# Kernel tuning notes

Measured on AMD Instinct MI355X. Metric: run time of the kernel, lower is better.

The kernel has to match this reference:

```python
import jax, jax.numpy as jnp
import numpy as np


def setup_inputs() -> dict:
    key = jax.random.key(0)
    k1, k2, k3, k4 = jax.random.split(key, 4)
    B, I, P, F = 4096, 1024, 512, 2048
    x = jax.random.normal(k1, (B, I), dtype=jnp.float32)
    # params initialized like torch.rand(...)*2-1 (uniform in [-1,1])
    features = jax.random.uniform(k2, (F, I), dtype=jnp.float32, minval=-1.0, maxval=1.0)
    prototypes = jax.random.uniform(k3, (P, I), dtype=jnp.float32, minval=-1.0, maxval=1.0)
    # scalars: torch inits to zeros; use small nonzero values so output/grads are informative
    abt = jax.random.normal(k4, (3,), dtype=jnp.float32) * 0.1
    alpha = abt[0:1]
    beta = abt[1:2]
    theta = abt[2:3]
    return {"x": x, "features": features, "prototypes": prototypes,
            "alpha": alpha, "beta": beta, "theta": theta}


def reference(x, features, prototypes, alpha, beta, theta):
    # x: [b, i], features: [f, i], prototypes: [p, i]
    # Original einsums broadcast over p but the projection is p-independent:
    xf = x @ features.T            # [b, f]
    pf = prototypes @ features.T   # [p, f]
    x_pres = jax.nn.relu(xf)       # [b, f]
    p_pres = jax.nn.relu(pf)       # [p, f]
    # common[b,p]       = sum_f xf*pf*relu(xf)*relu(pf)
    # x_distinct[b,p]   = sum_f xf*relu(xf)*(1-relu(pf))
    # p_distinct[b,p]   = sum_f pf*relu(pf)*(1-relu(xf))
    a = xf * x_pres                # [b, f]
    c = pf * p_pres                # [p, f]
    common = a @ c.T                                   # [b, p]
    x_distinctive = a @ (1.0 - p_pres).T               # [b, p]
    p_distinctive = (1.0 - x_pres) @ c.T               # [b, p]
    return theta * common - alpha * x_distinctive - beta * p_distinctive
```

## Files before the change

kernel.cpp:

```cpp
#include <hip/hip_runtime.h>
#include <cstdint>

typedef __attribute__((ext_vector_type(8))) short bf16x8;
typedef __attribute__((ext_vector_type(16))) float f32x16;
typedef __attribute__((ext_vector_type(4))) float f4;
typedef __attribute__((ext_vector_type(8))) unsigned short u16x8;
typedef unsigned short u16;


__device__ __forceinline__ u16 f2bf(float f) {
  uint32_t u = __builtin_bit_cast(uint32_t, f);
  u += 0x7fffu + ((u >> 16) & 1u);
  return (u16)(u >> 16);
}

__device__ __forceinline__ float bf2f(u16 h) {
  return __builtin_bit_cast(float, (uint32_t)h << 16);
}

__device__ __forceinline__ void async_cp16(const void* g, void* l) {
  __builtin_amdgcn_global_load_lds(
      (const __attribute__((address_space(1))) uint32_t*)g,
      (__attribute__((address_space(3))) uint32_t*)l, 16, 0, 0);
}

__global__ __launch_bounds__(256) void cast3(
    const float* __restrict__ x, const float* __restrict__ f,
    const float* __restrict__ p, u16* __restrict__ dst,
    int n1, int n2, int n3) {
  int i = (blockIdx.x * 256 + threadIdx.x) * 8;
  const float* src;
  int local;
  if (i < n1) { src = x; local = i; }
  else if (i < n1 + n2) { src = f; local = i - n1; }
  else if (i < n1 + n2 + n3) { src = p; local = i - n1 - n2; }
  else return;
  f4 a = *(const f4*)(src + local);
  f4 b = *(const f4*)(src + local + 4);
  u16x8 o;
  o[0] = f2bf(a.x); o[1] = f2bf(a.y); o[2] = f2bf(a.z); o[3] = f2bf(a.w);
  o[4] = f2bf(b.x); o[5] = f2bf(b.y); o[6] = f2bf(b.z); o[7] = f2bf(b.w);
  *(u16x8*)(dst + i) = o;
}


__device__ __forceinline__ void stage_tile(
    const u16* __restrict__ A, const u16* __restrict__ B, int K,
    int k0, int tid, u16* L) {
  constexpr int TM = 128, TN = 128;
  const int wave = tid >> 6;
  #pragma unroll
  for (int it = 0; it < TM / 32; ++it) {
    int c = it * 256 + tid;
    int row = c >> 3, pc = c & 7;
    int gc = pc ^ (row & 7);
    async_cp16(A + (size_t)row * K + (k0 + gc * 8),
               &L[(it * 256 + wave * 64) * 8]);
  }
  #pragma unroll
  for (int it = 0; it < TN / 32; ++it) {
    int c = it * 256 + tid;
    int row = c >> 3, pc = c & 7;
    int gc = pc ^ (row & 7);
    async_cp16(B + (size_t)row * K + (k0 + gc * 8),
               &L[TM * 64 + (it * 256 + wave * 64) * 8]);
  }
}

__device__ __forceinline__ void compute_tile(
    const u16* L, int lane, int wrow, int wcol, f32x16 (&acc)[2][2]) {
  constexpr int TM = 128;
  #pragma unroll
  for (int s = 0; s < 4; ++s) {
    const int h = s * 2 + (lane >> 5);
    bf16x8 bfr[2], afr[2];
    #pragma unroll
    for (int j = 0; j < 2; ++j) {
      const int rb = wcol * 64 + j * 32 + (lane & 31);
      bfr[j] = *(const bf16x8*)&L[TM * 64 + (rb * 8 + (h ^ (rb & 7))) * 8];
    }
    #pragma unroll
    for (int i = 0; i < 2; ++i) {
      const int ra = wrow * 64 + i * 32 + (lane & 31);
      afr[i] = *(const bf16x8*)&L[(ra * 8 + (h ^ (ra & 7))) * 8];
    }
    #pragma unroll
    for (int i = 0; i < 2; ++i)
      #pragma unroll
      for (int j = 0; j < 2; ++j)
        acc[i][j] = __builtin_amdgcn_mfma_f32_32x32x16_bf16(
            afr[i], bfr[j], acc[i][j], 0, 0, 0);
  }
}

__device__ __forceinline__ void mainloop(
    const u16* __restrict__ A, const u16* __restrict__ B, int K,
    int kbeg, int kend, int tid, u16* lds, f32x16 (&acc)[2][2]) {
  constexpr int BK = 64;
  constexpr int BUF = 16384;
  const int lane = tid & 63;
  const int wave = tid >> 6;
  const int wrow = wave >> 1, wcol = wave & 1;

  stage_tile(A, B, K, kbeg, tid, lds);
  int cur = 0;
  for (int k0 = kbeg; k0 < kend; k0 += BK) {
    if (k0 + BK < kend) {
      stage_tile(A, B, K, k0 + BK, tid, lds + (cur ^ 1) * BUF);
      asm volatile("s_waitcnt vmcnt(8)" ::: "memory");
    } else {
      asm volatile("s_waitcnt vmcnt(0)" ::: "memory");
    }
    __builtin_amdgcn_s_barrier();
    compute_tile(lds + cur * BUF, lane, wrow, wcol, acc);
    __builtin_amdgcn_s_barrier();
    cur ^= 1;
  }
}

__device__ __forceinline__ void mainloop_sb(
    const u16* __restrict__ A, const u16* __restrict__ B, int K,
    int kbeg, int kend, int tid, u16* lds, f32x16 (&acc)[2][2]) {
  constexpr int BK = 64;
  const int lane = tid & 63;
  const int wave = tid >> 6;
  const int wrow = wave >> 1, wcol = wave & 1;

  for (int k0 = kbeg; k0 < kend; k0 += BK) {
    stage_tile(A, B, K, k0, tid, lds);
    __syncthreads();
    compute_tile(lds, lane, wrow, wcol, acc);
    __syncthreads();
  }
}


__global__ __launch_bounds__(256) void gemm12(
    const u16* __restrict__ xb, const u16* __restrict__ pb,
    const u16* __restrict__ fb, u16* __restrict__ Acat, u16* __restrict__ Bcat,
    const float* __restrict__ alpha, const float* __restrict__ beta,
    const float* __restrict__ theta) {
  constexpr int TM = 128, K = 1024, N = 2048;
  constexpr int TSTRIDE = 136;
  __shared__ u16 lds[32768];

  const int tid = threadIdx.x;
  const int lane = tid & 63;
  const int wave = tid >> 6;
  const int wrow = wave >> 1, wcol = wave & 1;

  const int bid = blockIdx.x;
  const int xcd = bid & 7, slot = bid >> 3;
  const int xt = (xcd & 3) * 9 + (slot >> 3);
  const int yt = (xcd >> 2) * 8 + (slot & 7);

  const int bm_all = xt * TM;
  const int bn = yt * 128;
  const bool is_x = bm_all < 4096;
  const u16* A = is_x ? xb + (size_t)bm_all * K : pb + (size_t)(bm_all - 4096) * K;
  const u16* B = fb + (size_t)bn * K;

  f32x16 acc[2][2] = {};
  mainloop(A, B, K, 0, K, tid, lds, acc);

  float th = 0.f, al = 0.f, be = 0.f;
  if (!is_x) { th = theta[0]; al = alpha[0]; be = beta[0]; }
  u16* dst = is_x ? Acat : Bcat;
  const int rowbase = is_x ? bm_all : bm_all - 4096;
  const int rquad = 4 * (lane >> 5);

  #pragma unroll
  for (int half = 0; half < 2; ++half) {
    __syncthreads();
    #pragma unroll
    for (int i = 0; i < 2; ++i) {
      #pragma unroll
      for (int j = 0; j < 2; ++j) {
        const int cl = wcol * 64 + j * 32 + (lane & 31);
        #pragma unroll
        for (int r = 0; r < 16; ++r) {
          const int rl = wrow * 64 + i * 32 + (r & 3) + 8 * (r >> 2) + rquad;
          float v = acc[i][j][r];
          float pres = v > 0.f ? v : 0.f;
          float o;
          if (is_x) o = half == 0 ? v * pres : 1.f - pres;
          else {
            float cc = v * pres;
            o = half == 0 ? th * cc - al * (1.f - pres) : -be * cc;
          }
          lds[rl * TSTRIDE + cl] = f2bf(o);
        }
      }
    }
    __syncthreads();
    #pragma unroll
    for (int v = 0; v < 8; ++v) {
      const int rl = v * 16 + (tid >> 4);
      const int c8 = (tid & 15) * 8;
      u16x8 vec = *(const u16x8*)&lds[rl * TSTRIDE + c8];
      *(u16x8*)&dst[(size_t)(rowbase + rl) * (2 * N) + bn + c8 + half * N] = vec;
    }
  }
}

__global__ __launch_bounds__(256) void gemm3(
    const u16* __restrict__ Acat, const u16* __restrict__ Bcat,
    u16* __restrict__ part) {
  constexpr int TM = 128, TN = 128, K = 4096, KSPLIT = 8;
  __shared__ u16 lds[16384];

  const int tid = threadIdx.x;

  const int bid = blockIdx.x;
  const int bz = bid & 7;
  const int slot = bid >> 3;
  const int bxt = slot & 31;
  const int byt = slot >> 5;

  const int bm = bxt * TM;
  const int bn = byt * TN;
  const int kbeg = bz * (K / KSPLIT);
  const int kend = kbeg + (K / KSPLIT);

  f32x16 acc[2][2] = {};
  mainloop_sb(Acat + (size_t)bm * K, Bcat + (size_t)bn * K, K, kbeg, kend,
              tid, lds, acc);

  const size_t pbase = ((size_t)bz * 128 + byt * 32 + bxt) * 16384;
  #pragma unroll
  for (int i = 0; i < 2; ++i)
    #pragma unroll
    for (int j = 0; j < 2; ++j)
      #pragma unroll
      for (int h = 0; h < 2; ++h) {
        u16x8 o;
        #pragma unroll
        for (int e = 0; e < 8; ++e) o[e] = f2bf(acc[i][j][h * 8 + e]);
        *(u16x8*)&part[pbase + (size_t)(i * 4 + j * 2 + h) * 2048 + tid * 8] = o;
      }
}

__global__ __launch_bounds__(256) void reduce4(
    const u16* __restrict__ part, float* __restrict__ out) {
  constexpr int N = 512;
  const int tid = threadIdx.x;
  const int lane = tid & 63;
  const int wave = tid >> 6;
  const int wrow = wave >> 1, wcol = wave & 1;
  const int tileId = blockIdx.x >> 3;
  const int q = blockIdx.x & 7;
  const int bm = (tileId & 31) * 128;
  const int bn = (tileId >> 5) * 128;

  float v[8] = {};
  #pragma unroll
  for (int z = 0; z < 8; ++z) {
    u16x8 u = *(const u16x8*)&part[((size_t)z * 128 + tileId) * 16384 +
                                   (size_t)q * 2048 + tid * 8];
    #pragma unroll
    for (int e = 0; e < 8; ++e) v[e] += bf2f(u[e]);
  }
  const int i = q >> 2, j = (q >> 1) & 1, h = q & 1;
  const int gc = bn + wcol * 64 + j * 32 + (lane & 31);
  const int grb = bm + wrow * 64 + i * 32 + 4 * (lane >> 5);
  #pragma unroll
  for (int e = 0; e < 8; ++e) {
    const int reg = h * 8 + e;
    out[(size_t)(grb + (reg & 3) + 8 * (reg >> 2)) * N + gc] = v[e];
  }
}

extern "C" void kernel_launch(void* const* d_in, const int* in_sizes, int n_in,
                              void* d_out, int out_size, void* d_ws, size_t ws_size,
                              hipStream_t stream) {
  const float* x     = (const float*)d_in[0];
  const float* feat  = (const float*)d_in[1];
  const float* proto = (const float*)d_in[2];
  const float* alpha = (const float*)d_in[3];
  const float* beta  = (const float*)d_in[4];
  const float* theta = (const float*)d_in[5];
  float* out = (float*)d_out;

  constexpr int Bb = 4096, Ii = 1024, Pp = 512, Ff = 2048;

  char* ws = (char*)d_ws;
  u16* xb   = (u16*)ws;
  u16* fb   = xb + (size_t)Bb * Ii;
  u16* pb   = fb + (size_t)Ff * Ii;
  size_t r0 = 33554432;
  u16* Acat = (u16*)(ws + r0);
  u16* Bcat = Acat + (size_t)Bb * 2 * Ff;
  u16* part = Bcat + (size_t)Pp * 2 * Ff;

  const int n1 = Bb * Ii, n2 = Ff * Ii, n3 = Pp * Ii;
  cast3<<<((n1 + n2 + n3) / 8 + 255) / 256, 256, 0, stream>>>(
      x, feat, proto, xb, n1, n2, n3);

  gemm12<<<576, 256, 0, stream>>>(xb, pb, fb, Acat, Bcat, alpha, beta, theta);

  gemm3<<<1024, 256, 0, stream>>>(Acat, Bcat, part);

  reduce4<<<1024, 256, 0, stream>>>(part, out);
}
```

Measured before the change: 148.2 us.

## Enlarge gemm3 tiles to 256x256 with 8 waves and double-buffered async staging

The final GEMM moves from 128x128 tiles with 4 waves and a single-buffered loop to 256x256 tiles with 8 waves. Each wave computes a 128x64 subtile, and global-to-LDS loads are double-buffered asynchronously so they overlap compute. The partial-sum layout and the reduce kernel are updated to match. The aim is more operand reuse and less global traffic per FLOP, at the cost of only 256 blocks, which may underfill the CUs, plus heavy LDS use (128KB) and more register pressure.

```diff
diff --git a/kernel.cpp b/kernel.cpp
--- a/kernel.cpp
+++ b/kernel.cpp
@@ -118,19 +118,76 @@
   }
 }
 
-__device__ __forceinline__ void mainloop_sb(
+
+__device__ __forceinline__ void stage_tile256(
     const u16* __restrict__ A, const u16* __restrict__ B, int K,
-    int kbeg, int kend, int tid, u16* lds, f32x16 (&acc)[2][2]) {
+    int k0, int tid, u16* L) {
+  const int wave = tid >> 6;
+  #pragma unroll
+  for (int it = 0; it < 4; ++it) {
+    int c = it * 512 + tid;
+    int row = c >> 3, pc = c & 7;
+    int gc = pc ^ (row & 7);
+    async_cp16(A + (size_t)row * K + (k0 + gc * 8),
+               &L[(it * 512 + wave * 64) * 8]);
+  }
+  #pragma unroll
+  for (int it = 0; it < 4; ++it) {
+    int c = it * 512 + tid;
+    int row = c >> 3, pc = c & 7;
+    int gc = pc ^ (row & 7);
+    async_cp16(B + (size_t)row * K + (k0 + gc * 8),
+               &L[16384 + (it * 512 + wave * 64) * 8]);
+  }
+}
+
+__device__ __forceinline__ void compute_tile256(
+    const u16* L, int lane, int wrow, int wcol, f32x16 (&acc)[4][2]) {
+  #pragma unroll
+  for (int s = 0; s < 4; ++s) {
+    const int h = s * 2 + (lane >> 5);
+    bf16x8 bfr[2], afr[4];
+    #pragma unroll
+    for (int j = 0; j < 2; ++j) {
+      const int rb = wcol * 64 + j * 32 + (lane & 31);
+      bfr[j] = *(const bf16x8*)&L[16384 + (rb * 8 + (h ^ (rb & 7))) * 8];
+    }
+    #pragma unroll
+    for (int i = 0; i < 4; ++i) {
+      const int ra = wrow * 128 + i * 32 + (lane & 31);
+      afr[i] = *(const bf16x8*)&L[(ra * 8 + (h ^ (ra & 7))) * 8];
+    }
+    #pragma unroll
+    for (int i = 0; i < 4; ++i)
+      #pragma unroll
+      for (int j = 0; j < 2; ++j)
+        acc[i][j] = __builtin_amdgcn_mfma_f32_32x32x16_bf16(
+            afr[i], bfr[j], acc[i][j], 0, 0, 0);
+  }
+}
+
+__device__ __forceinline__ void mainloop256(
+    const u16* __restrict__ A, const u16* __restrict__ B, int K,
+    int kbeg, int kend, int tid, u16* lds, f32x16 (&acc)[4][2]) {
   constexpr int BK = 64;
+  constexpr int BUF = 32768;
   const int lane = tid & 63;
   const int wave = tid >> 6;
-  const int wrow = wave >> 1, wcol = wave & 1;
-
+  const int wrow = wave >> 2, wcol = wave & 3;
+
+  stage_tile256(A, B, K, kbeg, tid, lds);
+  int cur = 0;
   for (int k0 = kbeg; k0 < kend; k0 += BK) {
-    stage_tile(A, B, K, k0, tid, lds);
-    __syncthreads();
-    compute_tile(lds, lane, wrow, wcol, acc);
-    __syncthreads();
+    if (k0 + BK < kend) {
+      stage_tile256(A, B, K, k0 + BK, tid, lds + (cur ^ 1) * BUF);
+      asm volatile("s_waitcnt vmcnt(8)" ::: "memory");
+    } else {
+      asm volatile("s_waitcnt vmcnt(0)" ::: "memory");
+    }
+    __builtin_amdgcn_s_barrier();
+    compute_tile256(lds + cur * BUF, lane, wrow, wcol, acc);
+    __builtin_amdgcn_s_barrier();
+    cur ^= 1;
   }
 }
 
@@ -203,32 +260,32 @@
   }
 }
 
-__global__ __launch_bounds__(256) void gemm3(
+__global__ __launch_bounds__(512) void gemm3(
     const u16* __restrict__ Acat, const u16* __restrict__ Bcat,
     u16* __restrict__ part) {
-  constexpr int TM = 128, TN = 128, K = 4096, KSPLIT = 8;
-  __shared__ u16 lds[16384];
+  constexpr int K = 4096, KSPLIT = 8;
+  __shared__ u16 lds[65536];
 
   const int tid = threadIdx.x;
-
   const int bid = blockIdx.x;
   const int bz = bid & 7;
   const int slot = bid >> 3;
-  const int bxt = slot & 31;
-  const int byt = slot >> 5;
-
-  const int bm = bxt * TM;
-  const int bn = byt * TN;
+  const int bxt = slot & 15;
+  const int byt = slot >> 4;
+
+  const int bm = bxt * 256;
+  const int bn = byt * 256;
   const int kbeg = bz * (K / KSPLIT);
   const int kend = kbeg + (K / KSPLIT);
 
-  f32x16 acc[2][2] = {};
-  mainloop_sb(Acat + (size_t)bm * K, Bcat + (size_t)bn * K, K, kbeg, kend,
+  f32x16 acc[4][2] = {};
+  mainloop256(Acat + (size_t)bm * K, Bcat + (size_t)bn * K, K, kbeg, kend,
               tid, lds, acc);
 
-  const size_t pbase = ((size_t)bz * 128 + byt * 32 + bxt) * 16384;
-  #pragma unroll
-  for (int i = 0; i < 2; ++i)
+  const int tileId = byt * 16 + bxt;
+  const size_t pbase = ((size_t)bz * 32 + tileId) * 65536;
+  #pragma unroll
+  for (int i = 0; i < 4; ++i)
     #pragma unroll
     for (int j = 0; j < 2; ++j)
       #pragma unroll
@@ -236,33 +293,33 @@
         u16x8 o;
         #pragma unroll
         for (int e = 0; e < 8; ++e) o[e] = f2bf(acc[i][j][h * 8 + e]);
-        *(u16x8*)&part[pbase + (size_t)(i * 4 + j * 2 + h) * 2048 + tid * 8] = o;
+        *(u16x8*)&part[pbase + (size_t)(i * 4 + j * 2 + h) * 4096 + tid * 8] = o;
       }
 }
 
-__global__ __launch_bounds__(256) void reduce4(
+__global__ __launch_bounds__(512) void reduce4(
     const u16* __restrict__ part, float* __restrict__ out) {
   constexpr int N = 512;
   const int tid = threadIdx.x;
   const int lane = tid & 63;
   const int wave = tid >> 6;
-  const int wrow = wave >> 1, wcol = wave & 1;
-  const int tileId = blockIdx.x >> 3;
-  const int q = blockIdx.x & 7;
-  const int bm = (tileId & 31) * 128;
-  const int bn = (tileId >> 5) * 128;
+  const int wrow = wave >> 2, wcol = wave & 3;
+  const int tileId = blockIdx.x >> 4;
+  const int q = blockIdx.x & 15;
+  const int bm = (tileId & 15) * 256;
+  const int bn = (tileId >> 4) * 256;
 
   float v[8] = {};
   #pragma unroll
   for (int z = 0; z < 8; ++z) {
-    u16x8 u = *(const u16x8*)&part[((size_t)z * 128 + tileId) * 16384 +
-                                   (size_t)q * 2048 + tid * 8];
+    u16x8 u = *(const u16x8*)&part[((size_t)z * 32 + tileId) * 65536 +
+                                   (size_t)q * 4096 + tid * 8];
     #pragma unroll
     for (int e = 0; e < 8; ++e) v[e] += bf2f(u[e]);
   }
   const int i = q >> 2, j = (q >> 1) & 1, h = q & 1;
   const int gc = bn + wcol * 64 + j * 32 + (lane & 31);
-  const int grb = bm + wrow * 64 + i * 32 + 4 * (lane >> 5);
+  const int grb = bm + wrow * 128 + i * 32 + 4 * (lane >> 5);
   #pragma unroll
   for (int e = 0; e < 8; ++e) {
     const int reg = h * 8 + e;
@@ -298,7 +355,7 @@
 
   gemm12<<<576, 256, 0, stream>>>(xb, pb, fb, Acat, Bcat, alpha, beta, theta);
 
-  gemm3<<<1024, 256, 0, stream>>>(Acat, Bcat, part);
-
-  reduce4<<<1024, 256, 0, stream>>>(part, out);
-}
+  gemm3<<<256, 512, 0, stream>>>(Acat, Bcat, part);
+
+  reduce4<<<512, 512, 0, stream>>>(part, out);
+}
```

After: 138.2 us. 1.07x faster.
